# Performance work log

Measured on AMD Instinct MI355X. Metric: run time of the kernel, lower is better.

The kernel has to match this reference:

```python
import jax, jax.numpy as jnp
import numpy as np

B, T = 2048, 8
IN_DIM, OUT_DIM, E = 1024, 4096, 12


def setup_inputs() -> dict:
    key = jax.random.key(0)
    k = jax.random.split(key, 6)
    s = 1.0 / np.sqrt(IN_DIM)
    sg = 1.0 / np.sqrt(OUT_DIM)
    return {
        "x": jax.random.normal(k[0], (B, 1, IN_DIM), dtype=jnp.float32),
        "t": jax.random.normal(k[1], (B, T, OUT_DIM), dtype=jnp.float32),
        "W": jax.random.uniform(k[2], (E, IN_DIM, OUT_DIM), dtype=jnp.float32, minval=-s, maxval=s),
        "b": jax.random.uniform(k[3], (E, OUT_DIM), dtype=jnp.float32, minval=-s, maxval=s),
        "Wg": jax.random.uniform(k[4], (OUT_DIM, E), dtype=jnp.float32, minval=-sg, maxval=sg),
        "bg": jax.random.uniform(k[5], (E,), dtype=jnp.float32, minval=-sg, maxval=sg),
    }


def reference(x, t, W, b, Wg, bg):
    # x: [B,1,in], t: [B,T,out], W: [E,in,out], b: [E,out], Wg: [out,E], bg: [E]
    x_flat = x[:, 0, :]                                   # [B,in]
    t_mean = t.mean(axis=1)                               # [B,out]
    gate_logits = t_mean @ Wg + bg                        # [B,E]
    top1 = jnp.argmax(gate_logits, axis=-1)               # [B]
    # Dense per-expert linear, then select the top-1 expert's row per token.
    all_out = jnp.einsum('bi,eio->beo', x_flat, W) + b    # [B,E,out]
    out = all_out[jnp.arange(x.shape[0]), top1]           # [B,out]
    return out[:, None, :]                                # [B,1,out]
```

## Files before the change

kernel.cpp:

```cpp
#include <hip/hip_runtime.h>
#include <hip/hip_bf16.h>

#define B_ROWS  2048
#define T_DIM   8
#define IN_DIM  1024
#define OUT_DIM 4096
#define NE      12

#define M_TILE 128
#define N_TILE 128
#define K_STEP 32
#define NSTEP  (IN_DIM / K_STEP)
#define PACK_TILES 2

typedef __attribute__((ext_vector_type(8))) short short8;
typedef __attribute__((ext_vector_type(4))) float f32x4;

union S8U { short8 s; unsigned u[4]; };

__device__ __forceinline__ unsigned cvt2(float a, float b) {
  __hip_bfloat162 h = __float22bfloat162_rn(make_float2(a, b));
  union { __hip_bfloat162 h; unsigned u; } c; c.h = h;
  return c.u;
}

__device__ __forceinline__ void barrier_lgkm() {
  asm volatile("s_waitcnt lgkmcnt(0)" ::: "memory");
  __builtin_amdgcn_s_barrier();
}

__device__ __forceinline__ void gload_lds16(const void* g, void* l) {
  __builtin_amdgcn_global_load_lds(
      (const __attribute__((address_space(1))) void*)g,
      (__attribute__((address_space(3))) void*)l, 16, 0, 0);
}

__global__ __launch_bounds__(256) void wg_transpose(
    const float* __restrict__ Wg, float* __restrict__ wgt)
{
  const int c = blockIdx.x * 256 + threadIdx.x;
  #pragma unroll
  for (int e = 0; e < NE; ++e)
    wgt[(size_t)e * OUT_DIM + c] = Wg[(size_t)c * NE + e];
}

__global__ __launch_bounds__(256) void gate_kernel(
    const float* __restrict__ t, const float* __restrict__ wgt,
    const float* __restrict__ bg, int* __restrict__ counts,
    int* __restrict__ rowlist)
{
  const int b   = blockIdx.x;
  const int tid = threadIdx.x;
  const float* tb = t + (size_t)b * T_DIM * OUT_DIM;

  float4 m[4];
  #pragma unroll
  for (int it = 0; it < 4; ++it) {
    const int c = (tid + it * 256) * 4;
    float4 s = make_float4(0.f, 0.f, 0.f, 0.f);
    #pragma unroll
    for (int tt = 0; tt < T_DIM; ++tt) {
      const float4 v = *(const float4*)(tb + (size_t)tt * OUT_DIM + c);
      s.x += v.x; s.y += v.y; s.z += v.z; s.w += v.w;
    }
    m[it] = make_float4(s.x * 0.125f, s.y * 0.125f, s.z * 0.125f, s.w * 0.125f);
  }

  float part[NE];
  #pragma unroll
  for (int e = 0; e < NE; ++e) {
    float acc = 0.f;
    #pragma unroll
    for (int it = 0; it < 4; ++it) {
      const int c = (tid + it * 256) * 4;
      const float4 w = *(const float4*)(wgt + (size_t)e * OUT_DIM + c);
      acc += m[it].x * w.x; acc += m[it].y * w.y;
      acc += m[it].z * w.z; acc += m[it].w * w.w;
    }
    part[e] = acc;
  }

  double d[NE];
  #pragma unroll
  for (int e = 0; e < NE; ++e) d[e] = (double)part[e];
  #pragma unroll
  for (int off = 32; off > 0; off >>= 1) {
    #pragma unroll
    for (int e = 0; e < NE; ++e) d[e] += __shfl_down(d[e], off, 64);
  }

  __shared__ double wsred[4][NE];
  const int lane = tid & 63, wave = tid >> 6;
  if (lane == 0) {
    #pragma unroll
    for (int e = 0; e < NE; ++e) wsred[wave][e] = d[e];
  }
  __syncthreads();

  if (tid == 0) {
    double best = -1e300; int bi = 0;
    #pragma unroll
    for (int e = 0; e < NE; ++e) {
      const double v = wsred[0][e] + wsred[1][e] + wsred[2][e] + wsred[3][e] + (double)bg[e];
      if (v > best) { best = v; bi = e; }
    }
    const int pos = atomicAdd(&counts[bi], 1);
    rowlist[bi * B_ROWS + pos] = b;
  }
}

__global__ __launch_bounds__(256) void gate_fallback(
    const float* __restrict__ t, const float* __restrict__ Wg,
    const float* __restrict__ bg, int* __restrict__ counts,
    int* __restrict__ rowlist)
{
  const int b   = blockIdx.x;
  const int tid = threadIdx.x;
  const float* tb = t + (size_t)b * T_DIM * OUT_DIM;

  float part[NE];
  #pragma unroll
  for (int e = 0; e < NE; ++e) part[e] = 0.f;
  #pragma unroll
  for (int it = 0; it < 4; ++it) {
    const int c = (tid + it * 256) * 4;
    float4 s = make_float4(0.f, 0.f, 0.f, 0.f);
    #pragma unroll
    for (int tt = 0; tt < T_DIM; ++tt) {
      const float4 v = *(const float4*)(tb + (size_t)tt * OUT_DIM + c);
      s.x += v.x; s.y += v.y; s.z += v.z; s.w += v.w;
    }
    const float mm[4] = { s.x * 0.125f, s.y * 0.125f, s.z * 0.125f, s.w * 0.125f };
    #pragma unroll
    for (int j = 0; j < 4; ++j) {
      const float* wg = Wg + (size_t)(c + j) * NE;
      #pragma unroll
      for (int e = 0; e < NE; ++e) part[e] += mm[j] * wg[e];
    }
  }
  double d[NE];
  #pragma unroll
  for (int e = 0; e < NE; ++e) d[e] = (double)part[e];
  #pragma unroll
  for (int off = 32; off > 0; off >>= 1) {
    #pragma unroll
    for (int e = 0; e < NE; ++e) d[e] += __shfl_down(d[e], off, 64);
  }
  __shared__ double wsred[4][NE];
  const int lane = tid & 63, wave = tid >> 6;
  if (lane == 0) {
    #pragma unroll
    for (int e = 0; e < NE; ++e) wsred[wave][e] = d[e];
  }
  __syncthreads();
  if (tid == 0) {
    double best = -1e300; int bi = 0;
    #pragma unroll
    for (int e = 0; e < NE; ++e) {
      const double v = wsred[0][e] + wsred[1][e] + wsred[2][e] + wsred[3][e] + (double)bg[e];
      if (v > best) { best = v; bi = e; }
    }
    const int pos = atomicAdd(&counts[bi], 1);
    rowlist[bi * B_ROWS + pos] = b;
  }
}

__global__ __launch_bounds__(256) void pack_x(
    const float* __restrict__ x, const int* __restrict__ counts,
    const int* __restrict__ rowlist, short8* __restrict__ pxa)
{
  const int e   = blockIdx.x;
  const int rt  = blockIdx.y;
  const int it  = blockIdx.z;
  const int cnt = counts[e];
  const int row0 = rt * M_TILE;
  if (row0 >= cnt) return;
  const int* rl = rowlist + e * B_ROWS;
  const int tid = threadIdx.x;
  const int sg = (tid >> 4) & 3, slr = tid & 15, smb = tid >> 6;

  int g0 = row0 + smb * 16 + slr;        g0 = g0 < cnt ? g0 : cnt - 1;
  int g1 = row0 + (smb + 4) * 16 + slr;  g1 = g1 < cnt ? g1 : cnt - 1;
  const float* xp0 = x + (size_t)rl[g0] * IN_DIM + sg * 8 + it * K_STEP;
  const float* xp1 = x + (size_t)rl[g1] * IN_DIM + sg * 8 + it * K_STEP;

  const float4 a = *(const float4*)xp0, b = *(const float4*)(xp0 + 4);
  const float4 c = *(const float4*)xp1, d = *(const float4*)(xp1 + 4);
  S8U v0, v1;
  v0.u[0] = cvt2(a.x, a.y); v0.u[1] = cvt2(a.z, a.w);
  v0.u[2] = cvt2(b.x, b.y); v0.u[3] = cvt2(b.z, b.w);
  v1.u[0] = cvt2(c.x, c.y); v1.u[1] = cvt2(c.z, c.w);
  v1.u[2] = cvt2(d.x, d.y); v1.u[3] = cvt2(d.z, d.w);

  short8* dst = pxa + ((size_t)(e * PACK_TILES + rt) * NSTEP + it) * 512;
  dst[tid]       = v0.s;
  dst[tid + 256] = v1.s;
}

__global__ __launch_bounds__(256) void expert_gemm_packed(
    const float* __restrict__ W, const float* __restrict__ bias,
    const int* __restrict__ counts, const int* __restrict__ rowlist,
    const short8* __restrict__ pxa, float* __restrict__ out)
{
  const int e    = blockIdx.z;
  const int cnt  = counts[e];
  const int row0 = blockIdx.y * M_TILE;
  if (row0 >= cnt) return;
  const int c0   = blockIdx.x * N_TILE;
  const int* rl  = rowlist + e * B_ROWS;

  __shared__ short8 xa[2][512];
  __shared__ short8 wb[2][512];

  const int tid  = threadIdx.x;
  const int lane = tid & 63;
  const int wave = tid >> 6;
  const int sg = (tid >> 4) & 3, slr = tid & 15, smb = tid >> 6;

  const float* wp = W + (size_t)e * IN_DIM * OUT_DIM
                      + (size_t)(sg * 8) * OUT_DIM + c0 + smb * 16 + slr;

  const short8* at = pxa + (size_t)(e * PACK_TILES + blockIdx.y) * NSTEP * 512
                   + wave * 128 + lane;

  const int wm = (wave >> 1) * 64, wn = (wave & 1) * 64;
  const int abase = (wave >> 1) * 256, bbase = (wave & 1) * 256;

  f32x4 acc[4][4];
  #pragma unroll
  for (int m = 0; m < 4; ++m)
    #pragma unroll
    for (int n = 0; n < 4; ++n)
      #pragma unroll
      for (int q = 0; q < 4; ++q) acc[m][n][q] = 0.f;

  float w0[8], w1[8];

#define W_ISSUE(K)                                                      \
  {                                                                     \
    const float* p = wp + (size_t)(K) * OUT_DIM;                        \
    _Pragma("unroll")                                                   \
    for (int j = 0; j < 8; ++j) {                                       \
      w0[j] = p[(size_t)j * OUT_DIM];                                   \
      w1[j] = p[(size_t)j * OUT_DIM + 64];                              \
    }                                                                   \
  }

  W_ISSUE(0);
  gload_lds16(at,      &xa[0][wave * 128]);
  gload_lds16(at + 64, &xa[0][wave * 128 + 64]);
  __builtin_amdgcn_sched_barrier(0);

  #pragma unroll 2
  for (int it = 0; it < NSTEP; ++it) {
    const int buf = it & 1;

    S8U bv0, bv1;
    #pragma unroll
    for (int q = 0; q < 4; ++q) {
      bv0.u[q] = cvt2(w0[2 * q], w0[2 * q + 1]);
      bv1.u[q] = cvt2(w1[2 * q], w1[2 * q + 1]);
    }

    const int itn = (it + 1 < NSTEP) ? it + 1 : 0;
    W_ISSUE(itn * K_STEP);

    wb[buf][tid]       = bv0.s;
    wb[buf][tid + 256] = bv1.s;

    asm volatile("s_waitcnt vmcnt(16) lgkmcnt(0)" ::: "memory");
    __builtin_amdgcn_s_barrier();

    gload_lds16(at + (size_t)itn * 512,      &xa[buf ^ 1][wave * 128]);
    gload_lds16(at + (size_t)itn * 512 + 64, &xa[buf ^ 1][wave * 128 + 64]);
    __builtin_amdgcn_sched_barrier(0);

    short8 af[4], bf[4];
    #pragma unroll
    for (int m = 0; m < 4; ++m) af[m] = xa[buf][abase + m * 64 + lane];
    #pragma unroll
    for (int n = 0; n < 4; ++n) bf[n] = wb[buf][bbase + n * 64 + lane];
    #pragma unroll
    for (int m = 0; m < 4; ++m)
      #pragma unroll
      for (int n = 0; n < 4; ++n)
        acc[m][n] = __builtin_amdgcn_mfma_f32_16x16x32_bf16(af[m], bf[n], acc[m][n], 0, 0, 0);
  }
#undef W_ISSUE

  const int lr = lane & 15;
  const int lq = (lane >> 4) * 4;
  float bcol[4];
  #pragma unroll
  for (int n = 0; n < 4; ++n)
    bcol[n] = bias[e * OUT_DIM + c0 + wn + n * 16 + lr];

  #pragma unroll
  for (int m = 0; m < 4; ++m) {
    #pragma unroll
    for (int r = 0; r < 4; ++r) {
      const int gidx = row0 + wm + m * 16 + lq + r;
      if (gidx >= cnt) continue;
      const int grow = rl[gidx];
      float* orow = out + (size_t)grow * OUT_DIM;
      #pragma unroll
      for (int n = 0; n < 4; ++n) {
        const int col = c0 + wn + n * 16 + lr;
        orow[col] = acc[m][n][r] + bcol[n];
      }
    }
  }
}

__global__ __launch_bounds__(256) void expert_gemm_legacy(
    const float* __restrict__ x, const float* __restrict__ W,
    const float* __restrict__ bias, const int* __restrict__ counts,
    const int* __restrict__ rowlist, float* __restrict__ out, int y_off)
{
  const int e    = blockIdx.z;
  const int cnt  = counts[e];
  const int row0 = (blockIdx.y + y_off) * M_TILE;
  if (row0 >= cnt) return;
  const int c0   = blockIdx.x * N_TILE;
  const int* rl  = rowlist + e * B_ROWS;

  __shared__ short8 xa[2][512];
  __shared__ short8 wb[2][512];

  const int tid  = threadIdx.x;
  const int lane = tid & 63;
  const int wave = tid >> 6;
  const int sg  = (tid >> 4) & 3;
  const int slr = tid & 15;
  const int smb = tid >> 6;

  int arow0, arow1;
  {
    const int g0 = row0 + smb * 16 + slr;
    const int g1 = row0 + (smb + 4) * 16 + slr;
    arow0 = rl[g0 < cnt ? g0 : cnt - 1];
    arow1 = rl[g1 < cnt ? g1 : cnt - 1];
  }
  const float* xp0 = x + (size_t)arow0 * IN_DIM + sg * 8;
  const float* xp1 = x + (size_t)arow1 * IN_DIM + sg * 8;
  const float* wp  = W + (size_t)e * IN_DIM * OUT_DIM
                       + (size_t)(sg * 8) * OUT_DIM + c0 + smb * 16 + slr;

  const int wm = (wave >> 1) * 64;
  const int wn = (wave & 1) * 64;
  const int abase = (wave >> 1) * 256;
  const int bbase = (wave & 1) * 256;

  f32x4 acc[4][4];
  #pragma unroll
  for (int m = 0; m < 4; ++m)
    #pragma unroll
    for (int n = 0; n < 4; ++n)
      #pragma unroll
      for (int q = 0; q < 4; ++q) acc[m][n][q] = 0.f;

  float4 a0lo, a0hi, a1lo, a1hi;
  float w0[8], w1[8];

#define ISSUE_LOADS(K)                                                  \
  {                                                                     \
    a0lo = *(const float4*)(xp0 + (K));                                 \
    a0hi = *(const float4*)(xp0 + (K) + 4);                             \
    a1lo = *(const float4*)(xp1 + (K));                                 \
    a1hi = *(const float4*)(xp1 + (K) + 4);                             \
    const float* p = wp + (size_t)(K) * OUT_DIM;                        \
    _Pragma("unroll")                                                   \
    for (int j = 0; j < 8; ++j) {                                       \
      w0[j] = p[(size_t)j * OUT_DIM];                                   \
      w1[j] = p[(size_t)j * OUT_DIM + 64];                              \
    }                                                                   \
  }

  ISSUE_LOADS(0);

  for (int it = 0; it < NSTEP; ++it) {
    S8U av0, av1, bv0, bv1;
    av0.u[0] = cvt2(a0lo.x, a0lo.y); av0.u[1] = cvt2(a0lo.z, a0lo.w);
    av0.u[2] = cvt2(a0hi.x, a0hi.y); av0.u[3] = cvt2(a0hi.z, a0hi.w);
    av1.u[0] = cvt2(a1lo.x, a1lo.y); av1.u[1] = cvt2(a1lo.z, a1lo.w);
    av1.u[2] = cvt2(a1hi.x, a1hi.y); av1.u[3] = cvt2(a1hi.z, a1hi.w);
    #pragma unroll
    for (int q = 0; q < 4; ++q) {
      bv0.u[q] = cvt2(w0[2 * q], w0[2 * q + 1]);
      bv1.u[q] = cvt2(w1[2 * q], w1[2 * q + 1]);
    }

    if (it + 1 < NSTEP) ISSUE_LOADS((it + 1) * K_STEP);

    const int buf = it & 1;
    xa[buf][tid]       = av0.s;
    xa[buf][tid + 256] = av1.s;
    wb[buf][tid]       = bv0.s;
    wb[buf][tid + 256] = bv1.s;
    barrier_lgkm();

    short8 af[4], bf[4];
    #pragma unroll
    for (int m = 0; m < 4; ++m) af[m] = xa[buf][abase + m * 64 + lane];
    #pragma unroll
    for (int n = 0; n < 4; ++n) bf[n] = wb[buf][bbase + n * 64 + lane];
    #pragma unroll
    for (int m = 0; m < 4; ++m)
      #pragma unroll
      for (int n = 0; n < 4; ++n)
        acc[m][n] = __builtin_amdgcn_mfma_f32_16x16x32_bf16(af[m], bf[n], acc[m][n], 0, 0, 0);
  }
#undef ISSUE_LOADS

  const int lr = lane & 15;
  const int lq = (lane >> 4) * 4;
  float bcol[4];
  #pragma unroll
  for (int n = 0; n < 4; ++n)
    bcol[n] = bias[e * OUT_DIM + c0 + wn + n * 16 + lr];

  #pragma unroll
  for (int m = 0; m < 4; ++m) {
    #pragma unroll
    for (int r = 0; r < 4; ++r) {
      const int gidx = row0 + wm + m * 16 + lq + r;
      if (gidx >= cnt) continue;
      const int grow = rl[gidx];
      float* orow = out + (size_t)grow * OUT_DIM;
      #pragma unroll
      for (int n = 0; n < 4; ++n) {
        const int col = c0 + wn + n * 16 + lr;
        orow[col] = acc[m][n][r] + bcol[n];
      }
    }
  }
}

extern "C" void kernel_launch(void* const* d_in, const int* in_sizes, int n_in,
                              void* d_out, int out_size, void* d_ws, size_t ws_size,
                              hipStream_t stream) {
  (void)in_sizes; (void)n_in; (void)out_size;
  const float* x  = (const float*)d_in[0];
  const float* t  = (const float*)d_in[1];
  const float* W  = (const float*)d_in[2];
  const float* bb = (const float*)d_in[3];
  const float* Wg = (const float*)d_in[4];
  const float* bg = (const float*)d_in[5];
  float* out = (float*)d_out;

  char*  base    = (char*)d_ws;
  int*   counts  = (int*)base;
  int*   rowlist = (int*)(base + 64);
  float* wgt     = (float*)(base + 98368);
  short8* pxa    = (short8*)(base + 295936);
  const size_t need_wgt  = 98368 + 196608;
  const size_t need_pack = 295936 + (size_t)NE * PACK_TILES * NSTEP * 512 * 16;

  hipMemsetAsync(counts, 0, 64, stream);
  if (ws_size >= need_wgt) {
    wg_transpose<<<OUT_DIM / 256, 256, 0, stream>>>(Wg, wgt);
    gate_kernel<<<B_ROWS, 256, 0, stream>>>(t, wgt, bg, counts, rowlist);
  } else {
    gate_fallback<<<B_ROWS, 256, 0, stream>>>(t, Wg, bg, counts, rowlist);
  }

  if (ws_size >= need_pack) {
    pack_x<<<dim3(NE, PACK_TILES, NSTEP), 256, 0, stream>>>(x, counts, rowlist, pxa);
    expert_gemm_packed<<<dim3(OUT_DIM / N_TILE, PACK_TILES, NE), 256, 0, stream>>>(
        W, bb, counts, rowlist, pxa, out);
    expert_gemm_legacy<<<dim3(OUT_DIM / N_TILE, B_ROWS / M_TILE - PACK_TILES, NE),
                         256, 0, stream>>>(x, W, bb, counts, rowlist, out, PACK_TILES);
  } else {
    expert_gemm_legacy<<<dim3(OUT_DIM / N_TILE, B_ROWS / M_TILE, NE),
                         256, 0, stream>>>(x, W, bb, counts, rowlist, out, 0);
  }
}
```

Baseline: 163.2 us.

## Pre-pack expert weights to bf16 tiles and stream them via direct-to-LDS loads

Adds a pack_w kernel that converts every expert weight matrix to bf16, laid out tile by tile, into a large workspace buffer on each call. A new expert_gemm_dma kernel then loads both the activation and weight tiles straight into LDS with async global-to-LDS copies instead of converting fp32 weights in registers. Its flattened block index is swizzled so that blocks for the same expert are grouped. The aim is to take weight conversion and register staging out of the GEMM's inner loop. The cost is an extra full pass over all weights (fp32 read plus bf16 write) on every call, and the path needs roughly 100MB of workspace or it falls back to the old kernels.

```diff
diff --git a/kernel.cpp b/kernel.cpp
--- a/kernel.cpp
+++ b/kernel.cpp
@@ -12,6 +12,7 @@
 #define K_STEP 32
 #define NSTEP  (IN_DIM / K_STEP)
 #define PACK_TILES 2
+#define NCB    (OUT_DIM / N_TILE)
 
 typedef __attribute__((ext_vector_type(8))) short short8;
 typedef __attribute__((ext_vector_type(4))) float f32x4;
@@ -197,6 +198,135 @@
   dst[tid + 256] = v1.s;
 }
 
+__global__ __launch_bounds__(256) void pack_w(
+    const float* __restrict__ W, short8* __restrict__ pwb)
+{
+  const int cb = blockIdx.x;
+  const int it = blockIdx.y;
+  const int e  = blockIdx.z;
+  const int tid = threadIdx.x;
+  const int sg = (tid >> 4) & 3, slr = tid & 15, smb = tid >> 6;
+
+  const float* p0 = W + (size_t)e * IN_DIM * OUT_DIM
+                      + (size_t)(it * K_STEP + sg * 8) * OUT_DIM
+                      + cb * N_TILE + smb * 16 + slr;
+  const float* p1 = p0 + 64;
+
+  float w0[8], w1[8];
+  #pragma unroll
+  for (int j = 0; j < 8; ++j) {
+    w0[j] = p0[(size_t)j * OUT_DIM];
+    w1[j] = p1[(size_t)j * OUT_DIM];
+  }
+  S8U v0, v1;
+  #pragma unroll
+  for (int q = 0; q < 4; ++q) {
+    v0.u[q] = cvt2(w0[2 * q], w0[2 * q + 1]);
+    v1.u[q] = cvt2(w1[2 * q], w1[2 * q + 1]);
+  }
+  short8* dst = pwb + ((size_t)(e * NCB + cb) * NSTEP + it) * 512;
+  dst[tid]       = v0.s;
+  dst[tid + 256] = v1.s;
+}
+
+__global__ __launch_bounds__(256) void expert_gemm_dma(
+    const float* __restrict__ bias, const int* __restrict__ counts,
+    const int* __restrict__ rowlist, const short8* __restrict__ pxa,
+    const short8* __restrict__ pwb, float* __restrict__ out)
+{
+  const int bid = blockIdx.x;
+  const int wk  = (bid & 7) * 96 + (bid >> 3);
+  const int e   = wk >> 6;
+  const int rem = wk & 63;
+  const int cb  = rem >> 1;
+  const int rt  = rem & 1;
+  const int cnt  = counts[e];
+  const int row0 = rt * M_TILE;
+  if (row0 >= cnt) return;
+  const int c0   = cb * N_TILE;
+  const int* rl  = rowlist + e * B_ROWS;
+
+  __shared__ short8 xa[2][512];
+  __shared__ short8 wb[2][512];
+
+  const int tid  = threadIdx.x;
+  const int lane = tid & 63;
+  const int wave = tid >> 6;
+
+  const short8* at = pxa + (size_t)(e * PACK_TILES + rt) * NSTEP * 512
+                   + wave * 128 + lane;
+  const short8* bt = pwb + (size_t)(e * NCB + cb) * NSTEP * 512
+                   + wave * 128 + lane;
+
+  const int wm = (wave >> 1) * 64, wn = (wave & 1) * 64;
+  const int abase = (wave >> 1) * 256, bbase = (wave & 1) * 256;
+
+  f32x4 acc[4][4];
+  #pragma unroll
+  for (int m = 0; m < 4; ++m)
+    #pragma unroll
+    for (int n = 0; n < 4; ++n)
+      #pragma unroll
+      for (int q = 0; q < 4; ++q) acc[m][n][q] = 0.f;
+
+#define DMA_STEP(IT, BUF)                                               \
+  {                                                                     \
+    gload_lds16(at + (size_t)(IT) * 512,      &xa[BUF][wave * 128]);    \
+    gload_lds16(at + (size_t)(IT) * 512 + 64, &xa[BUF][wave * 128 + 64]); \
+    gload_lds16(bt + (size_t)(IT) * 512,      &wb[BUF][wave * 128]);    \
+    gload_lds16(bt + (size_t)(IT) * 512 + 64, &wb[BUF][wave * 128 + 64]); \
+    __builtin_amdgcn_sched_barrier(0);                                  \
+  }
+
+  DMA_STEP(0, 0);
+
+  for (int it = 0; it < NSTEP; ++it) {
+    const int buf = it & 1;
+    const int itn = (it + 1) & (NSTEP - 1);
+    DMA_STEP(itn, buf ^ 1);
+
+    asm volatile("s_waitcnt vmcnt(4)" ::: "memory");
+    __builtin_amdgcn_s_barrier();
+
+    short8 af[4], bf[4];
+    #pragma unroll
+    for (int m = 0; m < 4; ++m) af[m] = xa[buf][abase + m * 64 + lane];
+    #pragma unroll
+    for (int n = 0; n < 4; ++n) bf[n] = wb[buf][bbase + n * 64 + lane];
+    #pragma unroll
+    for (int m = 0; m < 4; ++m)
+      #pragma unroll
+      for (int n = 0; n < 4; ++n)
+        acc[m][n] = __builtin_amdgcn_mfma_f32_16x16x32_bf16(af[m], bf[n], acc[m][n], 0, 0, 0);
+
+    __builtin_amdgcn_s_barrier();
+  }
+#undef DMA_STEP
+
+  const int lr = lane & 15;
+  const int lq = (lane >> 4) * 4;
+  float bcol[4];
+  #pragma unroll
+  for (int n = 0; n < 4; ++n)
+    bcol[n] = bias[e * OUT_DIM + c0 + wn + n * 16 + lr];
+
+  #pragma unroll
+  for (int m = 0; m < 4; ++m) {
+    #pragma unroll
+    for (int r = 0; r < 4; ++r) {
+      const int gidx = row0 + wm + m * 16 + lq + r;
+      if (gidx >= cnt) continue;
+      const int grow = rl[gidx];
+      float* orow = out + (size_t)grow * OUT_DIM;
+      #pragma unroll
+      for (int n = 0; n < 4; ++n) {
+        const int col = c0 + wn + n * 16 + lr;
+        orow[col] = acc[m][n][r] + bcol[n];
+      }
+    }
+  }
+}
+
 __global__ __launch_bounds__(256) void expert_gemm_packed(
     const float* __restrict__ W, const float* __restrict__ bias,
     const int* __restrict__ counts, const int* __restrict__ rowlist,
@@ -219,7 +349,6 @@
 
   const float* wp = W + (size_t)e * IN_DIM * OUT_DIM
                       + (size_t)(sg * 8) * OUT_DIM + c0 + smb * 16 + slr;
-
   const short8* at = pxa + (size_t)(e * PACK_TILES + blockIdx.y) * NSTEP * 512
                    + wave * 128 + lane;
 
@@ -254,14 +383,12 @@
   #pragma unroll 2
   for (int it = 0; it < NSTEP; ++it) {
     const int buf = it & 1;
-
     S8U bv0, bv1;
     #pragma unroll
     for (int q = 0; q < 4; ++q) {
       bv0.u[q] = cvt2(w0[2 * q], w0[2 * q + 1]);
       bv1.u[q] = cvt2(w1[2 * q], w1[2 * q + 1]);
     }
-
     const int itn = (it + 1 < NSTEP) ? it + 1 : 0;
     W_ISSUE(itn * K_STEP);
 
@@ -453,10 +580,17 @@
   int*   rowlist = (int*)(base + 64);
   float* wgt     = (float*)(base + 98368);
   short8* pxa    = (short8*)(base + 295936);
-  const size_t need_wgt  = 98368 + 196608;
+  short8* pwb    = (short8*)(base + 6587392);
+  const size_t need_wgt  = 294976;
   const size_t need_pack = 295936 + (size_t)NE * PACK_TILES * NSTEP * 512 * 16;
+  const size_t need_pwb  = 6587392 + (size_t)NE * NCB * NSTEP * 512 * 16;
 
   hipMemsetAsync(counts, 0, 64, stream);
+
+  const bool has_pwb = (ws_size >= need_pwb);
+  if (has_pwb)
+    pack_w<<<dim3(NCB, NSTEP, NE), 256, 0, stream>>>(W, pwb);
+
   if (ws_size >= need_wgt) {
     wg_transpose<<<OUT_DIM / 256, 256, 0, stream>>>(Wg, wgt);
     gate_kernel<<<B_ROWS, 256, 0, stream>>>(t, wgt, bg, counts, rowlist);
@@ -464,14 +598,20 @@
     gate_fallback<<<B_ROWS, 256, 0, stream>>>(t, Wg, bg, counts, rowlist);
   }
 
-  if (ws_size >= need_pack) {
+  if (has_pwb) {
     pack_x<<<dim3(NE, PACK_TILES, NSTEP), 256, 0, stream>>>(x, counts, rowlist, pxa);
-    expert_gemm_packed<<<dim3(OUT_DIM / N_TILE, PACK_TILES, NE), 256, 0, stream>>>(
+    expert_gemm_dma<<<dim3(NE * NCB * PACK_TILES, 1, 1), 256, 0, stream>>>(
+        bb, counts, rowlist, pxa, pwb, out);
+    expert_gemm_legacy<<<dim3(NCB, B_ROWS / M_TILE - PACK_TILES, NE),
+                         256, 0, stream>>>(x, W, bb, counts, rowlist, out, PACK_TILES);
+  } else if (ws_size >= need_pack) {
+    pack_x<<<dim3(NE, PACK_TILES, NSTEP), 256, 0, stream>>>(x, counts, rowlist, pxa);
+    expert_gemm_packed<<<dim3(NCB, PACK_TILES, NE), 256, 0, stream>>>(
         W, bb, counts, rowlist, pxa, out);
-    expert_gemm_legacy<<<dim3(OUT_DIM / N_TILE, B_ROWS / M_TILE - PACK_TILES, NE),
+    expert_gemm_legacy<<<dim3(NCB, B_ROWS / M_TILE - PACK_TILES, NE),
                          256, 0, stream>>>(x, W, bb, counts, rowlist, out, PACK_TILES);
   } else {
-    expert_gemm_legacy<<<dim3(OUT_DIM / N_TILE, B_ROWS / M_TILE, NE),
+    expert_gemm_legacy<<<dim3(NCB, B_ROWS / M_TILE, NE),
                          256, 0, stream>>>(x, W, bb, counts, rowlist, out, 0);
   }
 }
```

New measurement: 183.2 us. +12.3%, slower.

## Merge both packed row tiles into one 512-thread block sharing W tile

Applied to the files above, without the earlier changes.

The packed expert GEMM now uses 8 waves per block, covering both 128-row tiles (256 rows) of an expert against a single 128-column W tile. Each fp32 W slab is loaded and converted to bf16 once per block instead of once per row tile. The grid becomes a flat 1D launch with a remapped block index that spreads experts and column blocks across XCDs. The trade-offs are larger blocks with lower per-thread W-load depth (vmcnt 8), and blocks still run full work when an expert has only a few rows.

```diff
diff --git a/kernel.cpp b/kernel.cpp
--- a/kernel.cpp
+++ b/kernel.cpp
@@ -12,6 +12,7 @@
 #define K_STEP 32
 #define NSTEP  (IN_DIM / K_STEP)
 #define PACK_TILES 2
+#define NCB    (OUT_DIM / N_TILE)
 
 typedef __attribute__((ext_vector_type(8))) short short8;
 typedef __attribute__((ext_vector_type(4))) float f32x4;
@@ -197,34 +198,37 @@
   dst[tid + 256] = v1.s;
 }
 
-__global__ __launch_bounds__(256) void expert_gemm_packed(
+__global__ __launch_bounds__(512) void expert_gemm8(
     const float* __restrict__ W, const float* __restrict__ bias,
     const int* __restrict__ counts, const int* __restrict__ rowlist,
     const short8* __restrict__ pxa, float* __restrict__ out)
 {
-  const int e    = blockIdx.z;
-  const int cnt  = counts[e];
-  const int row0 = blockIdx.y * M_TILE;
-  if (row0 >= cnt) return;
-  const int c0   = blockIdx.x * N_TILE;
-  const int* rl  = rowlist + e * B_ROWS;
-
-  __shared__ short8 xa[2][512];
+  const int bid = blockIdx.x;
+  const int wk  = (bid & 7) * 48 + (bid >> 3);
+  const int e   = wk >> 5;
+  const int cb  = wk & 31;
+  const int cnt = counts[e];
+  const int c0  = cb * N_TILE;
+  const int* rl = rowlist + e * B_ROWS;
+
+  __shared__ short8 xa[2][1024];
   __shared__ short8 wb[2][512];
 
   const int tid  = threadIdx.x;
   const int lane = tid & 63;
   const int wave = tid >> 6;
+
   const int sg = (tid >> 4) & 3, slr = tid & 15, smb = tid >> 6;
-
   const float* wp = W + (size_t)e * IN_DIM * OUT_DIM
                       + (size_t)(sg * 8) * OUT_DIM + c0 + smb * 16 + slr;
 
-  const short8* at = pxa + (size_t)(e * PACK_TILES + blockIdx.y) * NSTEP * 512
-                   + wave * 128 + lane;
-
-  const int wm = (wave >> 1) * 64, wn = (wave & 1) * 64;
-  const int abase = (wave >> 1) * 256, bbase = (wave & 1) * 256;
+  const short8* at = pxa + (size_t)(e * PACK_TILES + (wave >> 2)) * NSTEP * 512
+                   + (wave & 3) * 128 + lane;
+
+  const int wm = (wave >> 1) * 64;
+  const int wn = (wave & 1) * 64;
+  const int abase = (wave >> 2) * 512 + ((wave >> 1) & 1) * 256;
+  const int bbase = (wave & 1) * 256;
 
   f32x4 acc[4][4];
   #pragma unroll
@@ -234,46 +238,40 @@
       #pragma unroll
       for (int q = 0; q < 4; ++q) acc[m][n][q] = 0.f;
 
-  float w0[8], w1[8];
+  float w0[8];
 
 #define W_ISSUE(K)                                                      \
   {                                                                     \
     const float* p = wp + (size_t)(K) * OUT_DIM;                        \
     _Pragma("unroll")                                                   \
-    for (int j = 0; j < 8; ++j) {                                       \
-      w0[j] = p[(size_t)j * OUT_DIM];                                   \
-      w1[j] = p[(size_t)j * OUT_DIM + 64];                              \
-    }                                                                   \
+    for (int j = 0; j < 8; ++j) w0[j] = p[(size_t)j * OUT_DIM];         \
+  }
+#define A_DMA(IT, BUF)                                                  \
+  {                                                                     \
+    gload_lds16(at + (size_t)(IT) * 512,      &xa[BUF][wave * 128]);    \
+    gload_lds16(at + (size_t)(IT) * 512 + 64, &xa[BUF][wave * 128 + 64]); \
+    __builtin_amdgcn_sched_barrier(0);                                  \
   }
 
   W_ISSUE(0);
-  gload_lds16(at,      &xa[0][wave * 128]);
-  gload_lds16(at + 64, &xa[0][wave * 128 + 64]);
-  __builtin_amdgcn_sched_barrier(0);
-
-  #pragma unroll 2
+  A_DMA(0, 0);
+
   for (int it = 0; it < NSTEP; ++it) {
     const int buf = it & 1;
-
-    S8U bv0, bv1;
-    #pragma unroll
-    for (int q = 0; q < 4; ++q) {
-      bv0.u[q] = cvt2(w0[2 * q], w0[2 * q + 1]);
-      bv1.u[q] = cvt2(w1[2 * q], w1[2 * q + 1]);
-    }
-
-    const int itn = (it + 1 < NSTEP) ? it + 1 : 0;
+    const int itn = (it + 1) & (NSTEP - 1);
+
+    S8U bv;
+    #pragma unroll
+    for (int q = 0; q < 4; ++q)
+      bv.u[q] = cvt2(w0[2 * q], w0[2 * q + 1]);
+
     W_ISSUE(itn * K_STEP);
-
-    wb[buf][tid]       = bv0.s;
-    wb[buf][tid + 256] = bv1.s;
-
-    asm volatile("s_waitcnt vmcnt(16) lgkmcnt(0)" ::: "memory");
+    wb[buf][tid] = bv.s;
+
+    asm volatile("s_waitcnt vmcnt(8) lgkmcnt(0)" ::: "memory");
     __builtin_amdgcn_s_barrier();
 
-    gload_lds16(at + (size_t)itn * 512,      &xa[buf ^ 1][wave * 128]);
-    gload_lds16(at + (size_t)itn * 512 + 64, &xa[buf ^ 1][wave * 128 + 64]);
-    __builtin_amdgcn_sched_barrier(0);
+    A_DMA(itn, buf ^ 1);
 
     short8 af[4], bf[4];
     #pragma unroll
@@ -287,6 +285,7 @@
         acc[m][n] = __builtin_amdgcn_mfma_f32_16x16x32_bf16(af[m], bf[n], acc[m][n], 0, 0, 0);
   }
 #undef W_ISSUE
+#undef A_DMA
 
   const int lr = lane & 15;
   const int lq = (lane >> 4) * 4;
@@ -299,7 +298,7 @@
   for (int m = 0; m < 4; ++m) {
     #pragma unroll
     for (int r = 0; r < 4; ++r) {
-      const int gidx = row0 + wm + m * 16 + lq + r;
+      const int gidx = wm + m * 16 + lq + r;
       if (gidx >= cnt) continue;
       const int grow = rl[gidx];
       float* orow = out + (size_t)grow * OUT_DIM;
@@ -453,7 +452,7 @@
   int*   rowlist = (int*)(base + 64);
   float* wgt     = (float*)(base + 98368);
   short8* pxa    = (short8*)(base + 295936);
-  const size_t need_wgt  = 98368 + 196608;
+  const size_t need_wgt  = 294976;
   const size_t need_pack = 295936 + (size_t)NE * PACK_TILES * NSTEP * 512 * 16;
 
   hipMemsetAsync(counts, 0, 64, stream);
@@ -466,12 +465,12 @@
 
   if (ws_size >= need_pack) {
     pack_x<<<dim3(NE, PACK_TILES, NSTEP), 256, 0, stream>>>(x, counts, rowlist, pxa);
-    expert_gemm_packed<<<dim3(OUT_DIM / N_TILE, PACK_TILES, NE), 256, 0, stream>>>(
+    expert_gemm8<<<dim3(NE * NCB, 1, 1), 512, 0, stream>>>(
         W, bb, counts, rowlist, pxa, out);
-    expert_gemm_legacy<<<dim3(OUT_DIM / N_TILE, B_ROWS / M_TILE - PACK_TILES, NE),
+    expert_gemm_legacy<<<dim3(NCB, B_ROWS / M_TILE - PACK_TILES, NE),
                          256, 0, stream>>>(x, W, bb, counts, rowlist, out, PACK_TILES);
   } else {
-    expert_gemm_legacy<<<dim3(OUT_DIM / N_TILE, B_ROWS / M_TILE, NE),
+    expert_gemm_legacy<<<dim3(NCB, B_ROWS / M_TILE, NE),
                          256, 0, stream>>>(x, W, bb, counts, rowlist, out, 0);
   }
 }
```

Measured after the change: 140.8 us. 13.7% less time.
